# Performance work log

Measured on AMD Instinct MI355X. Metric: run time of the kernel, lower is better.

The kernel has to match this reference:

```python
import jax, jax.numpy as jnp
import numpy as np

SELF_MASK = 1e6  # large value added on the diagonal to exclude self-distance


def setup_inputs() -> dict:
    key = jax.random.key(0)
    # (B, N, 3) point cloud
    point_cloud = jax.random.normal(key, (4, 4096, 3), dtype=jnp.float32)
    return {"point_cloud": point_cloud}


def reference(point_cloud):
    B, N, _ = point_cloud.shape
    # Spread-of-radii term: variance (unbiased, matching torch.var default)
    # of distances to the per-cloud centroid.
    centroids = jnp.mean(point_cloud, axis=1, keepdims=True)          # (B,1,3)
    dists = jnp.linalg.norm(point_cloud - centroids, axis=2)          # (B,N)
    dist_variance = jnp.var(dists, axis=1, ddof=1)                    # (B,)

    # Pairwise squared distances via the gram expansion
    # ||x_i - x_j||^2 = ||x_i||^2 + ||x_j||^2 - 2 <x_i, x_j>
    # (avoids materializing the (B,N,N,3) difference tensor).
    sq = jnp.sum(point_cloud * point_cloud, axis=-1)                  # (B,N)
    gram = jnp.einsum('bnd,bmd->bnm', point_cloud, point_cloud)       # (B,N,N)
    pair_dist = jnp.maximum(sq[:, :, None] + sq[:, None, :] - 2.0 * gram, 0.0)
    pair_dist = pair_dist + jnp.eye(N, dtype=pair_dist.dtype) * SELF_MASK

    # Nearest-neighbor squared distance per point, then repulsion penalty.
    min_nn_dist = jnp.min(pair_dist, axis=2)                          # (B,N)
    nn_penalty = jnp.mean(jnp.exp(-5.0 * min_nn_dist))

    return jnp.mean(dist_variance) + nn_penalty
```

## Files before the change

kernel.cpp:

```cpp
#include <hip/hip_runtime.h>
#include <math.h>

#define NB    4
#define NPTS  4096
#define BN    (NB * NPTS)
#define TPB   1024
#define QPB   64
#define NBLK  (BN / QPB)
#define G     64
#define JG    (NPTS / G)
#define IT    4
#define QCOLS (QPB / IT)
#define NW    (TPB / 64)
#define PADIDX(i) ((i) + ((i) >> 6))

__device__ inline float wave_sum(float v) {
#pragma unroll
    for (int o = 32; o > 0; o >>= 1) v += __shfl_xor(v, o);
    return v;
}

__global__ __launch_bounds__(TPB) void fused_kernel(const float* __restrict__ pc,
                                                    float* __restrict__ bpart) {
    __shared__ float4 lpt[NPTS + G];
    __shared__ float  smin[NW][QPB];
    __shared__ float  scen[NW][3];

    int b    = blockIdx.x >> 6;
    int blkq = blockIdx.x & 63;
    int iq0  = blkq * QPB;
    const float* p = pc + (size_t)b * NPTS * 3;
    int t = threadIdx.x;
    int lane = t & 63, w = t >> 6;

    float sx = 0.f, sy = 0.f, sz = 0.f;
#pragma unroll
    for (int i = t; i < NPTS; i += TPB) {
        float x = p[3*i+0], y = p[3*i+1], z = p[3*i+2];
        lpt[PADIDX(i)] = make_float4(x, y, z, fmaf(x, x, fmaf(y, y, z * z)));
        sx += x; sy += y; sz += z;
    }
    sx = wave_sum(sx); sy = wave_sum(sy); sz = wave_sum(sz);
    if (lane == 0) { scen[w][0] = sx; scen[w][1] = sy; scen[w][2] = sz; }
    __syncthreads();

    int qcol = t & (QCOLS - 1);
    int g    = t >> 4;
    float ax[IT], ay[IT], az[IT], m[IT];
#pragma unroll
    for (int k = 0; k < IT; ++k) {
        int iq = iq0 + qcol * IT + k;
        float4 q = lpt[PADIDX(iq)];
        ax[k] = -2.f * q.x; ay[k] = -2.f * q.y; az[k] = -2.f * q.z;
        m[k] = 1e30f;
    }
    const float4* gp = &lpt[g * (JG + 1)];

    int gd = blkq;
    int wd = gd >> 2;
    if (w == wd) {
        int idl[IT];
#pragma unroll
        for (int k = 0; k < IT; ++k)
            idl[k] = (g == gd) ? (qcol * IT + k) : -1;
#pragma unroll 4
        for (int j = 0; j < JG; ++j) {
            float4 q = gp[j];
#pragma unroll
            for (int k = 0; k < IT; ++k) {
                float e = fmaf(ax[k], q.x, fmaf(ay[k], q.y, fmaf(az[k], q.z, q.w)));
                m[k] = fminf(m[k], (j == idl[k]) ? 1e30f : e);
            }
        }
    } else {
#pragma unroll 8
        for (int j = 0; j < JG; j += 2) {
            float4 q0 = gp[j], q1 = gp[j+1];
#pragma unroll
            for (int k = 0; k < IT; ++k) {
                float e0 = fmaf(ax[k], q0.x, fmaf(ay[k], q0.y, fmaf(az[k], q0.z, q0.w)));
                float e1 = fmaf(ax[k], q1.x, fmaf(ay[k], q1.y, fmaf(az[k], q1.z, q1.w)));
                m[k] = fminf(fminf(m[k], e0), e1);
            }
        }
    }

#pragma unroll
    for (int k = 0; k < IT; ++k) {
        m[k] = fminf(m[k], __shfl_xor(m[k], 16));
        m[k] = fminf(m[k], __shfl_xor(m[k], 32));
    }
    if (lane < QCOLS) {
#pragma unroll
        for (int k = 0; k < IT; ++k) smin[w][qcol * IT + k] = m[k];
    }
    __syncthreads();

    if (t < QPB) {
        float cx = 0.f, cy = 0.f, cz = 0.f;
#pragma unroll
        for (int ww = 0; ww < NW; ++ww) {
            cx += scen[ww][0]; cy += scen[ww][1]; cz += scen[ww][2];
        }
        cx *= (1.f / NPTS); cy *= (1.f / NPTS); cz *= (1.f / NPTS);

        float mm = smin[0][t];
#pragma unroll
        for (int ww = 1; ww < NW; ++ww) mm = fminf(mm, smin[ww][t]);

        int iq = iq0 + t;
        float4 q = lpt[PADIDX(iq)];
        float es = __expf(-5.f * fmaxf(q.w + mm, 0.f));

        float dx = q.x - cx, dy = q.y - cy, dz = q.z - cz;
        float d2 = fmaf(dx, dx, fmaf(dy, dy, dz * dz));
        float s1 = sqrtf(d2);

        es = wave_sum(es);
        float S1 = wave_sum(s1);
        float S2 = wave_sum(d2);
        if (t == 0) {
            bpart[blockIdx.x * 3 + 0] = S1;
            bpart[blockIdx.x * 3 + 1] = S2;
            bpart[blockIdx.x * 3 + 2] = es;
        }
    }
}

__global__ __launch_bounds__(256) void finish_kernel(const float* __restrict__ bpart,
                                                     float* __restrict__ out) {
    __shared__ float svar[NB], ses[NB];
    int t = threadIdx.x;
    int w = t >> 6;
    float s1 = bpart[t*3+0], s2 = bpart[t*3+1], es = bpart[t*3+2];
    s1 = wave_sum(s1); s2 = wave_sum(s2); es = wave_sum(es);
    if ((t & 63) == 0) {
        svar[w] = (s2 - s1 * s1 * (1.f / NPTS)) * (1.f / (NPTS - 1));
        ses[w]  = es;
    }
    __syncthreads();
    if (t == 0) {
        float vs = 0.f, et = 0.f;
#pragma unroll
        for (int bb = 0; bb < NB; ++bb) { vs += svar[bb]; et += ses[bb]; }
        out[0] = vs * (1.f / NB) + et * (1.f / BN);
    }
}

extern "C" void kernel_launch(void* const* d_in, const int* in_sizes, int n_in,
                              void* d_out, int out_size, void* d_ws, size_t ws_size,
                              hipStream_t stream) {
    const float* pc = (const float*)d_in[0];
    float* out   = (float*)d_out;
    float* bpart = (float*)d_ws;

    fused_kernel<<<NBLK, TPB, 0, stream>>>(pc, bpart);
    finish_kernel<<<1, 256, 0, stream>>>(bpart, out);
}
```

Baseline: 15.81 us.

## Halve block size to 512 threads with 32 queries per block, doubling grid

The fused nearest-neighbour kernel now launches 512 blocks of 512 threads, each handling 32 query points instead of 64. The j-range is split into 64-point groups, and the self-exclusion index, the cross-lane reduction and the finish kernel are adapted to the new layout. The finish kernel now combines two partials per cloud before computing the variance. The aim is more blocks for the 256 CUs and better occupancy. The cost is that every block still loads and preprocesses the full 4096-point cloud into LDS, so that redundant work doubles.

```diff
diff --git a/kernel.cpp b/kernel.cpp
--- a/kernel.cpp
+++ b/kernel.cpp
@@ -4,13 +4,13 @@
 #define NB    4
 #define NPTS  4096
 #define BN    (NB * NPTS)
-#define TPB   1024
-#define QPB   64
+#define TPB   512
+#define QPB   32
 #define NBLK  (BN / QPB)
-#define G     64
-#define JG    (NPTS / G)
 #define IT    4
 #define QCOLS (QPB / IT)
+#define G     (TPB / QCOLS)
+#define JG    (NPTS / G)
 #define NW    (TPB / 64)
 #define PADIDX(i) ((i) + ((i) >> 6))
 
@@ -20,14 +20,15 @@
     return v;
 }
 
-__global__ __launch_bounds__(TPB) void fused_kernel(const float* __restrict__ pc,
-                                                    float* __restrict__ bpart) {
+__global__ __launch_bounds__(TPB, 4) void fused_kernel(const float* __restrict__ pc,
+                                                       float* __restrict__ bpart) {
     __shared__ float4 lpt[NPTS + G];
     __shared__ float  smin[NW][QPB];
     __shared__ float  scen[NW][3];
 
-    int b    = blockIdx.x >> 6;
-    int blkq = blockIdx.x & 63;
+    int blk  = blockIdx.x;
+    int b    = blk >> 7;
+    int blkq = blk & 127;
     int iq0  = blkq * QPB;
     const float* p = pc + (size_t)b * NPTS * 3;
     int t = threadIdx.x;
@@ -45,7 +46,7 @@
     __syncthreads();
 
     int qcol = t & (QCOLS - 1);
-    int g    = t >> 4;
+    int g    = t >> 3;
     float ax[IT], ay[IT], az[IT], m[IT];
 #pragma unroll
     for (int k = 0; k < IT; ++k) {
@@ -56,13 +57,13 @@
     }
     const float4* gp = &lpt[g * (JG + 1)];
 
-    int gd = blkq;
-    int wd = gd >> 2;
+    int gd = blkq >> 1;
+    int wd = gd >> 3;
     if (w == wd) {
         int idl[IT];
 #pragma unroll
         for (int k = 0; k < IT; ++k)
-            idl[k] = (g == gd) ? (qcol * IT + k) : -1;
+            idl[k] = (g == gd) ? ((blkq & 1) * 32 + qcol * IT + k) : -1;
 #pragma unroll 4
         for (int j = 0; j < JG; ++j) {
             float4 q = gp[j];
@@ -87,6 +88,7 @@
 
 #pragma unroll
     for (int k = 0; k < IT; ++k) {
+        m[k] = fminf(m[k], __shfl_xor(m[k], 8));
         m[k] = fminf(m[k], __shfl_xor(m[k], 16));
         m[k] = fminf(m[k], __shfl_xor(m[k], 32));
     }
@@ -96,53 +98,56 @@
     }
     __syncthreads();
 
-    if (t < QPB) {
-        float cx = 0.f, cy = 0.f, cz = 0.f;
+    if (t < 64) {
+        float es = 0.f, s1v = 0.f, d2v = 0.f;
+        if (t < QPB) {
+            float cx = 0.f, cy = 0.f, cz = 0.f;
 #pragma unroll
-        for (int ww = 0; ww < NW; ++ww) {
-            cx += scen[ww][0]; cy += scen[ww][1]; cz += scen[ww][2];
+            for (int ww = 0; ww < NW; ++ww) {
+                cx += scen[ww][0]; cy += scen[ww][1]; cz += scen[ww][2];
+            }
+            cx *= (1.f / NPTS); cy *= (1.f / NPTS); cz *= (1.f / NPTS);
+
+            float mm = smin[0][t];
+#pragma unroll
+            for (int ww = 1; ww < NW; ++ww) mm = fminf(mm, smin[ww][t]);
+
+            int iq = iq0 + t;
+            float4 q = lpt[PADIDX(iq)];
+            es = __expf(-5.f * fmaxf(q.w + mm, 0.f));
+
+            float dx = q.x - cx, dy = q.y - cy, dz = q.z - cz;
+            d2v = fmaf(dx, dx, fmaf(dy, dy, dz * dz));
+            s1v = sqrtf(d2v);
         }
-        cx *= (1.f / NPTS); cy *= (1.f / NPTS); cz *= (1.f / NPTS);
-
-        float mm = smin[0][t];
-#pragma unroll
-        for (int ww = 1; ww < NW; ++ww) mm = fminf(mm, smin[ww][t]);
-
-        int iq = iq0 + t;
-        float4 q = lpt[PADIDX(iq)];
-        float es = __expf(-5.f * fmaxf(q.w + mm, 0.f));
-
-        float dx = q.x - cx, dy = q.y - cy, dz = q.z - cz;
-        float d2 = fmaf(dx, dx, fmaf(dy, dy, dz * dz));
-        float s1 = sqrtf(d2);
-
-        es = wave_sum(es);
-        float S1 = wave_sum(s1);
-        float S2 = wave_sum(d2);
+        es  = wave_sum(es);
+        float S1 = wave_sum(s1v);
+        float S2 = wave_sum(d2v);
         if (t == 0) {
-            bpart[blockIdx.x * 3 + 0] = S1;
-            bpart[blockIdx.x * 3 + 1] = S2;
-            bpart[blockIdx.x * 3 + 2] = es;
+            bpart[blk * 3 + 0] = S1;
+            bpart[blk * 3 + 1] = S2;
+            bpart[blk * 3 + 2] = es;
         }
     }
 }
 
-__global__ __launch_bounds__(256) void finish_kernel(const float* __restrict__ bpart,
+__global__ __launch_bounds__(512) void finish_kernel(const float* __restrict__ bpart,
                                                      float* __restrict__ out) {
-    __shared__ float svar[NB], ses[NB];
-    int t = threadIdx.x;
-    int w = t >> 6;
+    __shared__ float a1[NW * 1], a2[NW * 1], ae[NW * 1];
+    int t = threadIdx.x, w = t >> 6;
     float s1 = bpart[t*3+0], s2 = bpart[t*3+1], es = bpart[t*3+2];
     s1 = wave_sum(s1); s2 = wave_sum(s2); es = wave_sum(es);
-    if ((t & 63) == 0) {
-        svar[w] = (s2 - s1 * s1 * (1.f / NPTS)) * (1.f / (NPTS - 1));
-        ses[w]  = es;
-    }
+    if ((t & 63) == 0) { a1[w] = s1; a2[w] = s2; ae[w] = es; }
     __syncthreads();
     if (t == 0) {
         float vs = 0.f, et = 0.f;
 #pragma unroll
-        for (int bb = 0; bb < NB; ++bb) { vs += svar[bb]; et += ses[bb]; }
+        for (int bb = 0; bb < NB; ++bb) {
+            float S1 = a1[2*bb] + a1[2*bb+1];
+            float S2 = a2[2*bb] + a2[2*bb+1];
+            vs += (S2 - S1 * S1 * (1.f / NPTS)) * (1.f / (NPTS - 1));
+            et += ae[2*bb] + ae[2*bb+1];
+        }
         out[0] = vs * (1.f / NB) + et * (1.f / BN);
     }
 }
@@ -155,5 +160,5 @@
     float* bpart = (float*)d_ws;
 
     fused_kernel<<<NBLK, TPB, 0, stream>>>(pc, bpart);
-    finish_kernel<<<1, 256, 0, stream>>>(bpart, out);
+    finish_kernel<<<1, 512, 0, stream>>>(bpart, out);
 }
```

After: 16.74 us. +5.9%, slower.
